# Kernel tuning notes

Measured on AMD Instinct MI355X. Metric: run time of the kernel, lower is better.

Reference implementation:

```python
import jax, jax.numpy as jnp
import numpy as np

B, S, D = 4, 4096, 64
NEG = 1e31  # matches the torch module's -1e+31 masking constant


def setup_inputs() -> dict:
    key = jax.random.key(0)
    kq, kk, kv = jax.random.split(key, 3)
    return {
        "query": jax.random.normal(kq, (B, S, D), dtype=jnp.float32),
        "key": jax.random.normal(kk, (B, S, D), dtype=jnp.float32),
        "value": jax.random.normal(kv, (B, S, D), dtype=jnp.float32),
    }


def reference(query, key, value):
    # scores: [B, Sq, Sk]
    attn_weights = jnp.einsum("bqd,bkd->bqk", query, key)
    # NOTE: original subtracts the causal penalty BEFORE the sqrt(d) scaling
    Sq, Sk = query.shape[1], key.shape[1]
    causal_mask = jnp.triu(jnp.ones((Sq, Sk), dtype=attn_weights.dtype), k=1)
    attn_weights = attn_weights - causal_mask[None, :, :] * NEG
    attn_weights = attn_weights / np.sqrt(key.shape[-1]).astype(np.float32)
    attn_weights = jax.nn.softmax(attn_weights, axis=-1)
    # dropout p=0.0 -> identity on value
    attn_vec = jnp.einsum("bqk,bkd->bqd", attn_weights, value)
    return attn_vec, attn_weights
```

## Files before the change

kernel.cpp:

```cpp
#include <hip/hip_runtime.h>


#define SQ 4096
#define DD 64
#define NB 4
#define NEL (NB*SQ*DD)
#define PSTRIDE 4104

typedef __attribute__((ext_vector_type(4))) float f32x4;
typedef __attribute__((ext_vector_type(8))) __bf16 bf16x8;

__device__ __forceinline__ unsigned short f2bf(float f) {
  unsigned int u = __builtin_bit_cast(unsigned int, f);
  u = (u + 0x7FFFu + ((u >> 16) & 1u)) >> 16;
  return (unsigned short)u;
}

__device__ __forceinline__ bf16x8 ldfrag(const unsigned short* p) {
  uint4 u = *(const uint4*)p;
  return __builtin_bit_cast(bf16x8, u);
}

__device__ __forceinline__ float bf2f(unsigned short u) {
  return __builtin_bit_cast(float, (unsigned int)u << 16);
}

__global__ __launch_bounds__(256) void prep_kernel(
    const float* __restrict__ q, const float* __restrict__ k,
    const float* __restrict__ v, unsigned short* __restrict__ ws)
{
  unsigned short* qbf = ws;
  unsigned short* kbf = ws + (size_t)NEL;
  unsigned short* vt  = ws + 2*(size_t)NEL;
  const int bid = blockIdx.x;
  const int tid = threadIdx.x;
  if (bid < 1024) {
    const float* src = (bid < 512) ? q : k;
    unsigned short* dst = (bid < 512) ? qbf : kbf;
    const int base = (bid & 511) * 512 + tid;
#pragma unroll
    for (int i = 0; i < 2; ++i) {
      int idx = base + i * 256;
      float4 f = ((const float4*)src)[idx];
      ushort4 o;
      o.x = f2bf(f.x); o.y = f2bf(f.y); o.z = f2bf(f.z); o.w = f2bf(f.w);
      ((ushort4*)dst)[idx] = o;
    }
  } else {
    __shared__ unsigned short tile[64][66];
    const int t  = bid - 1024;
    const int bb = t >> 6;
    const int st = t & 63;
    const float* vb = v + (size_t)bb * SQ * DD + (size_t)st * 64 * DD;
    const int r  = tid >> 4;
    const int c4 = tid & 15;
#pragma unroll
    for (int j = 0; j < 4; ++j) {
      int row = r + j * 16;
      float4 f = ((const float4*)(vb + (size_t)row * DD))[c4];
      tile[row][c4 * 4 + 0] = f2bf(f.x);
      tile[row][c4 * 4 + 1] = f2bf(f.y);
      tile[row][c4 * 4 + 2] = f2bf(f.z);
      tile[row][c4 * 4 + 3] = f2bf(f.w);
    }
    __syncthreads();
    unsigned short* vtb = vt + (size_t)bb * DD * SQ;
#pragma unroll
    for (int j = 0; j < 4; ++j) {
      int d   = r + j * 16;
      int s0l = c4 * 4;
      ushort4 o;
      o.x = tile[s0l + 0][d];
      o.y = tile[s0l + 1][d];
      o.z = tile[s0l + 2][d];
      o.w = tile[s0l + 3][d];
      ((ushort4*)(vtb + (size_t)d * SQ + st * 64))[c4] = o;
    }
  }
}

__global__ __launch_bounds__(512, 2) void attn_kernel(
    const unsigned short* __restrict__ qbf,
    const unsigned short* __restrict__ kbf,
    const unsigned short* __restrict__ vtp,
    float* __restrict__ out_vec,
    float* __restrict__ out_w)
{
  __shared__ __align__(16) unsigned short Ps[16 * PSTRIDE];
  __shared__ float lred[8][4][4];
  __shared__ float inv_l_s[16];

  const int tid  = threadIdx.x;
  const int wave = tid >> 6;
  const int lane = tid & 63;
  const int l16  = lane & 15;
  const int quad = lane >> 4;

  const int bidx = blockIdx.x;
  const int b    = bidx & 3;
  const int qt   = 255 - (bidx >> 2);

  const unsigned short* Qb = qbf + (size_t)b * SQ * DD;
  const unsigned short* Kb = kbf + (size_t)b * SQ * DD;
  const unsigned short* Vt = vtp + (size_t)b * DD * SQ;
  float* Wb = out_w  + (size_t)b * SQ * SQ;
  float* Ob = out_vec + (size_t)b * SQ * DD;

  const int q0    = qt * 16;
  const int rowg0 = q0 + quad * 4;

  bf16x8 aQ0, aQ1;
  {
    const unsigned short* qrow = Qb + (size_t)(q0 + l16) * DD + quad * 8;
    aQ0 = ldfrag(qrow);
    aQ1 = ldfrag(qrow + 32);
  }

  const int nkt  = (qt >> 2) + 1;
  const int nch  = (nkt + 15) >> 4;
  const int nstp = nch << 3;
  const float SC = 0.125f * 1.4426950408889634f;
  const f32x4 zf = {0.f, 0.f, 0.f, 0.f};

  float lsum[4] = {0.f, 0.f, 0.f, 0.f};
  for (int st = wave; st < nstp; st += 8) {
    const int k0c = st * 128;
    if (k0c <= q0 + 15) {
#pragma unroll
      for (int h = 0; h < 2; ++h) {
        const int k0 = k0c + h * 64;
        f32x4 acc[4] = {zf, zf, zf, zf};
#pragma unroll
        for (int ct = 0; ct < 4; ++ct) {
          const unsigned short* krow = Kb + (size_t)(k0 + ct * 16 + l16) * DD + quad * 8;
          bf16x8 b0 = ldfrag(krow);
          bf16x8 b1 = ldfrag(krow + 32);
          acc[ct] = __builtin_amdgcn_mfma_f32_16x16x32_bf16(aQ0, b0, acc[ct], 0, 0, 0);
          acc[ct] = __builtin_amdgcn_mfma_f32_16x16x32_bf16(aQ1, b1, acc[ct], 0, 0, 0);
        }
#pragma unroll
        for (int ct = 0; ct < 4; ++ct) {
          const int colg = k0 + ct * 16 + l16;
#pragma unroll
          for (int r = 0; r < 4; ++r) {
            float tt = (colg <= rowg0 + r) ? acc[ct][r] * SC : -1e30f;
            float p  = __builtin_amdgcn_exp2f(tt);
            lsum[r] += p;
            Ps[(quad * 4 + r) * PSTRIDE + colg] =
                __builtin_bit_cast(unsigned short, (__bf16)p);
          }
        }
      }
    } else {
#pragma unroll
      for (int h = 0; h < 2; ++h)
#pragma unroll
        for (int ct = 0; ct < 4; ++ct)
#pragma unroll
          for (int r = 0; r < 4; ++r)
            Ps[(quad * 4 + r) * PSTRIDE + k0c + h * 64 + ct * 16 + l16] = 0;
    }
  }

#pragma unroll
  for (int r = 0; r < 4; ++r) {
    float v = lsum[r];
    v += __shfl_xor(v, 1);
    v += __shfl_xor(v, 2);
    v += __shfl_xor(v, 4);
    v += __shfl_xor(v, 8);
    lsum[r] = v;
  }
  if (l16 == 0) {
#pragma unroll
    for (int r = 0; r < 4; ++r) lred[wave][quad][r] = lsum[r];
  }
  __syncthreads();
  if (tid < 16) {
    float s = 0.f;
#pragma unroll
    for (int w = 0; w < 8; ++w) s += lred[w][tid >> 2][tid & 3];
    inv_l_s[tid] = 1.0f / s;
  }
  __syncthreads();

  f32x4 accO[4] = {zf, zf, zf, zf};
  const int r0 = 2 * wave;

  for (int ch = 0; ch < nch; ++ch) {
    const int c0 = ch << 10;
#pragma unroll
    for (int rr = 0; rr < 2; ++rr) {
      const int row = r0 + rr;
      const float invr = inv_l_s[row];
      const unsigned short* src = &Ps[row * PSTRIDE + c0];
      float* dst = Wb + (size_t)(q0 + row) * SQ + c0;
#pragma unroll
      for (int g = 0; g < 4; ++g) {
        ushort4 u = *(const ushort4*)(src + g * 256 + lane * 4);
        f32x4 o;
        o[0] = bf2f(u.x) * invr;
        o[1] = bf2f(u.y) * invr;
        o[2] = bf2f(u.z) * invr;
        o[3] = bf2f(u.w) * invr;
        *(f32x4*)(dst + g * 256 + lane * 4) = o;
      }
    }
    const int sb = c0 + wave * 128;
    if (sb <= q0 + 15) {
#pragma unroll
      for (int kk = 0; kk < 4; ++kk) {
        const int cb = sb + kk * 32 + quad * 8;
        bf16x8 aP = *(const bf16x8*)(&Ps[l16 * PSTRIDE + cb]);
#pragma unroll
        for (int ct = 0; ct < 4; ++ct) {
          const unsigned short* vrow = Vt + (size_t)(ct * 16 + l16) * SQ + cb;
          bf16x8 bv = ldfrag(vrow);
          accO[ct] = __builtin_amdgcn_mfma_f32_16x16x32_bf16(aP, bv, accO[ct], 0, 0, 0);
        }
      }
    }
  }

  float invq[4];
#pragma unroll
  for (int r = 0; r < 4; ++r) invq[r] = inv_l_s[quad * 4 + r];
  __syncthreads();
  float* stag = (float*)Ps;
  float* ow = stag + wave * 1024;
#pragma unroll
  for (int ct = 0; ct < 4; ++ct)
#pragma unroll
    for (int r = 0; r < 4; ++r)
      ow[(quad * 4 + r) * 64 + ct * 16 + l16] = accO[ct][r] * invq[r];
  __syncthreads();
#pragma unroll
  for (int i = 0; i < 2; ++i) {
    int idx = tid + i * 512;
    int row = idx >> 6, col = idx & 63;
    float s = 0.f;
#pragma unroll
    for (int w = 0; w < 8; ++w) s += stag[w * 1024 + row * 64 + col];
    Ob[(size_t)(q0 + row) * DD + col] = s;
  }

  const int zc0 = nch << 10;
  const int nz4 = (SQ - zc0) >> 2;
  if (nz4 > 0) {
    for (int r = 0; r < 16; ++r) {
      f32x4* zp = (f32x4*)(Wb + (size_t)(q0 + r) * SQ + zc0);
      for (int i = tid; i < nz4; i += 512)
        zp[i] = zf;
    }
  }
}

extern "C" void kernel_launch(void* const* d_in, const int* in_sizes, int n_in,
                              void* d_out, int out_size, void* d_ws, size_t ws_size,
                              hipStream_t stream) {
  const float* q = (const float*)d_in[0];
  const float* k = (const float*)d_in[1];
  const float* v = (const float*)d_in[2];
  float* out_vec = (float*)d_out;
  float* out_w   = out_vec + (size_t)NB * SQ * DD;
  unsigned short* ws = (unsigned short*)d_ws;

  hipLaunchKernelGGL(prep_kernel, dim3(1280), dim3(256), 0, stream, q, k, v, ws);
  hipLaunchKernelGGL(attn_kernel, dim3(1024), dim3(512), 0, stream,
                     ws, ws + (size_t)NEL, ws + 2 * (size_t)NEL,
                     out_vec, out_w);
}
```

Baseline: 312.2 us.

## Transpose QK MFMA operands, prefetch K tiles, and vectorize P stores

Swaps the MFMA operand order so each lane holds four consecutive key columns for one query row. This lets probabilities be packed and written to LDS as one 8-byte store, and it cuts the row-sum reduction from four shuffle chains to a single two-step reduction. K fragments for the next 64-key tile are loaded ahead of time into registers (double buffering) to hide global latency. The work unit changes from 128-key steps to 64-key tiles strided across waves. The extra K registers raise register pressure under the 512x2 launch bounds.

```diff
diff --git a/kernel.cpp b/kernel.cpp
--- a/kernel.cpp
+++ b/kernel.cpp
@@ -87,7 +87,7 @@
     float* __restrict__ out_w)
 {
   __shared__ __align__(16) unsigned short Ps[16 * PSTRIDE];
-  __shared__ float lred[8][4][4];
+  __shared__ float lredS[8][16];
   __shared__ float inv_l_s[16];
 
   const int tid  = threadIdx.x;
@@ -106,93 +106,107 @@
   float* Wb = out_w  + (size_t)b * SQ * SQ;
   float* Ob = out_vec + (size_t)b * SQ * DD;
 
-  const int q0    = qt * 16;
-  const int rowg0 = q0 + quad * 4;
+  const int q0   = qt * 16;
+  const int qrow = q0 + l16;
 
   bf16x8 aQ0, aQ1;
   {
-    const unsigned short* qrow = Qb + (size_t)(q0 + l16) * DD + quad * 8;
-    aQ0 = ldfrag(qrow);
-    aQ1 = ldfrag(qrow + 32);
-  }
-
-  const int nkt  = (qt >> 2) + 1;
-  const int nch  = (nkt + 15) >> 4;
-  const int nstp = nch << 3;
+    const unsigned short* qrp = Qb + (size_t)(q0 + l16) * DD + quad * 8;
+    aQ0 = ldfrag(qrp);
+    aQ1 = ldfrag(qrp + 32);
+  }
+
+  const int nkt = (qt >> 2) + 1;
+  const int nch = (nkt + 15) >> 4;
+  const int ntp = nch << 4;
+  const int lastlive = (q0 + 15) >> 6;
   const float SC = 0.125f * 1.4426950408889634f;
   const f32x4 zf = {0.f, 0.f, 0.f, 0.f};
 
-  float lsum[4] = {0.f, 0.f, 0.f, 0.f};
-  for (int st = wave; st < nstp; st += 8) {
-    const int k0c = st * 128;
-    if (k0c <= q0 + 15) {
-#pragma unroll
-      for (int h = 0; h < 2; ++h) {
-        const int k0 = k0c + h * 64;
+  float lsum = 0.f;
+  bf16x8 ka[8], kb[8];
+  {
+    int kt = wave;
+    if (kt <= lastlive) {
+#pragma unroll
+      for (int ct = 0; ct < 4; ++ct) {
+        const unsigned short* krow =
+            Kb + (size_t)(kt * 64 + ct * 16 + l16) * DD + quad * 8;
+        ka[2 * ct]     = ldfrag(krow);
+        ka[2 * ct + 1] = ldfrag(krow + 32);
+      }
+    }
+    for (; kt < ntp; kt += 8) {
+      const int ktn = kt + 8;
+      if (ktn <= lastlive) {
+#pragma unroll
+        for (int ct = 0; ct < 4; ++ct) {
+          const unsigned short* krow =
+              Kb + (size_t)(ktn * 64 + ct * 16 + l16) * DD + quad * 8;
+          kb[2 * ct]     = ldfrag(krow);
+          kb[2 * ct + 1] = ldfrag(krow + 32);
+        }
+      }
+      const int k0 = kt * 64;
+      if (kt <= lastlive) {
         f32x4 acc[4] = {zf, zf, zf, zf};
 #pragma unroll
         for (int ct = 0; ct < 4; ++ct) {
-          const unsigned short* krow = Kb + (size_t)(k0 + ct * 16 + l16) * DD + quad * 8;
-          bf16x8 b0 = ldfrag(krow);
-          bf16x8 b1 = ldfrag(krow + 32);
-          acc[ct] = __builtin_amdgcn_mfma_f32_16x16x32_bf16(aQ0, b0, acc[ct], 0, 0, 0);
-          acc[ct] = __builtin_amdgcn_mfma_f32_16x16x32_bf16(aQ1, b1, acc[ct], 0, 0, 0);
-        }
-#pragma unroll
-        for (int ct = 0; ct < 4; ++ct) {
-          const int colg = k0 + ct * 16 + l16;
-#pragma unroll
-          for (int r = 0; r < 4; ++r) {
-            float tt = (colg <= rowg0 + r) ? acc[ct][r] * SC : -1e30f;
-            float p  = __builtin_amdgcn_exp2f(tt);
-            lsum[r] += p;
-            Ps[(quad * 4 + r) * PSTRIDE + colg] =
-                __builtin_bit_cast(unsigned short, (__bf16)p);
-          }
-        }
-      }
-    } else {
-#pragma unroll
-      for (int h = 0; h < 2; ++h)
+          acc[ct] = __builtin_amdgcn_mfma_f32_16x16x32_bf16(ka[2 * ct],     aQ0, acc[ct], 0, 0, 0);
+          acc[ct] = __builtin_amdgcn_mfma_f32_16x16x32_bf16(ka[2 * ct + 1], aQ1, acc[ct], 0, 0, 0);
+        }
+#pragma unroll
+        for (int ct = 0; ct < 4; ++ct) {
+          const int colb = k0 + ct * 16 + quad * 4;
+          float p0 = __builtin_amdgcn_exp2f((colb + 0 <= qrow) ? acc[ct][0] * SC : -1e30f);
+          float p1 = __builtin_amdgcn_exp2f((colb + 1 <= qrow) ? acc[ct][1] * SC : -1e30f);
+          float p2 = __builtin_amdgcn_exp2f((colb + 2 <= qrow) ? acc[ct][2] * SC : -1e30f);
+          float p3 = __builtin_amdgcn_exp2f((colb + 3 <= qrow) ? acc[ct][3] * SC : -1e30f);
+          lsum += (p0 + p1) + (p2 + p3);
+          ushort4 pk;
+          pk.x = __builtin_bit_cast(unsigned short, (__bf16)p0);
+          pk.y = __builtin_bit_cast(unsigned short, (__bf16)p1);
+          pk.z = __builtin_bit_cast(unsigned short, (__bf16)p2);
+          pk.w = __builtin_bit_cast(unsigned short, (__bf16)p3);
+          *(ushort4*)&Ps[l16 * PSTRIDE + colb] = pk;
+        }
+#pragma unroll
+        for (int i = 0; i < 8; ++i) ka[i] = kb[i];
+      } else {
+        const ushort4 z4 = {0, 0, 0, 0};
 #pragma unroll
         for (int ct = 0; ct < 4; ++ct)
-#pragma unroll
-          for (int r = 0; r < 4; ++r)
-            Ps[(quad * 4 + r) * PSTRIDE + k0c + h * 64 + ct * 16 + l16] = 0;
-    }
-  }
-
-#pragma unroll
-  for (int r = 0; r < 4; ++r) {
-    float v = lsum[r];
-    v += __shfl_xor(v, 1);
-    v += __shfl_xor(v, 2);
-    v += __shfl_xor(v, 4);
-    v += __shfl_xor(v, 8);
-    lsum[r] = v;
-  }
-  if (l16 == 0) {
-#pragma unroll
-    for (int r = 0; r < 4; ++r) lred[wave][quad][r] = lsum[r];
+          *(ushort4*)&Ps[l16 * PSTRIDE + k0 + ct * 16 + quad * 4] = z4;
+      }
+    }
+  }
+
+  {
+    float v = lsum;
+    v += __shfl_xor(v, 16);
+    v += __shfl_xor(v, 32);
+    if (lane < 16) lredS[wave][lane] = v;
   }
   __syncthreads();
   if (tid < 16) {
     float s = 0.f;
 #pragma unroll
-    for (int w = 0; w < 8; ++w) s += lred[w][tid >> 2][tid & 3];
+    for (int w = 0; w < 8; ++w) s += lredS[w][tid];
     inv_l_s[tid] = 1.0f / s;
   }
   __syncthreads();
 
   f32x4 accO[4] = {zf, zf, zf, zf};
   const int r0 = 2 * wave;
+  const float invr0 = inv_l_s[r0];
+  const float invr1 = inv_l_s[r0 + 1];
 
   for (int ch = 0; ch < nch; ++ch) {
     const int c0 = ch << 10;
 #pragma unroll
     for (int rr = 0; rr < 2; ++rr) {
       const int row = r0 + rr;
-      const float invr = inv_l_s[row];
+      const float invr = rr ? invr1 : invr0;
       const unsigned short* src = &Ps[row * PSTRIDE + c0];
       float* dst = Wb + (size_t)(q0 + row) * SQ + c0;
 #pragma unroll
```

Result: no change. 311.0 us (-0.4%).
